# Performance work log

Hardware: AMD Instinct MI355X
Metric: run time of the kernel (lower is better)

The kernel has to match this reference:

```python
import jax, jax.numpy as jnp
import numpy as np

B, D, H, O, E, K = 16384, 3072, 128, 10, 8, 2


def setup_inputs() -> dict:
    key = jax.random.key(0)
    ks = jax.random.split(key, 9)
    s_d = 1.0 / np.sqrt(D)
    s_h = 1.0 / np.sqrt(H)
    return {
        "x": jax.random.normal(ks[0], (B, D), dtype=jnp.float32),
        "gate_w": jax.random.uniform(ks[1], (D, E), jnp.float32, -s_d, s_d),
        "gate_b": jnp.zeros((E,), jnp.float32),
        "w1": jax.random.uniform(ks[2], (E, D, H), jnp.float32, -s_d, s_d),
        "b1": jax.random.uniform(ks[3], (E, H), jnp.float32, -s_d, s_d),
        "w2": jax.random.uniform(ks[4], (E, H, H), jnp.float32, -s_h, s_h),
        "b2": jax.random.uniform(ks[5], (E, H), jnp.float32, -s_h, s_h),
        "w3": jax.random.uniform(ks[6], (E, H, O), jnp.float32, -s_h, s_h),
        "b3": jax.random.uniform(ks[7], (E, O), jnp.float32, -s_h, s_h),
    }


def reference(x, gate_w, gate_b, w1, b1, w2, b2, w3, b3):
    # Gate: scores [B, E]
    scores = x @ gate_w + gate_b
    _, topk_idx = jax.lax.top_k(scores, K)          # [B, K]
    mask = jax.nn.one_hot(topk_idx, E, dtype=scores.dtype).sum(axis=-2)  # [B, E] 0/1
    weights = jax.nn.softmax(scores, axis=-1) * mask
    weights = weights / (weights.sum(axis=-1, keepdims=True) + 1e-8)

    # Compute all experts (dropout is identity in eval mode)
    h1 = jax.nn.relu(jnp.einsum('bd,edh->beh', x, w1) + b1)   # [B, E, H]
    h2 = jax.nn.relu(jnp.einsum('beh,ehg->beg', h1, w2) + b2)  # [B, E, H]
    out = jnp.einsum('beh,eho->beo', h2, w3) + b3              # [B, E, O]

    y = jnp.einsum('be,beo->bo', weights, out)                 # [B, O]
    return y
```

## Files before the change

### kernel.cpp

```cpp
#include <hip/hip_runtime.h>
#include <hip/hip_bf16.h>

#define B_ROWS 16384
#define D_DIM  3072
#define H_DIM  128
#define O_DIM  10
#define E_NUM  8

typedef __hip_bfloat16 bf16;
typedef __attribute__((ext_vector_type(8))) short short8;
typedef __attribute__((ext_vector_type(4))) float floatx4;

__global__ void transpose_bf16_kernel(const float* __restrict__ in,
                                      bf16* __restrict__ out, int R, int C) {
    int e = blockIdx.z;
    const float* inp = in + (size_t)e * R * C;
    bf16* outp = out + (size_t)e * R * C;
    __shared__ float tile[32][33];
    int tx = threadIdx.x;
    int ty = threadIdx.y;
    int r0 = blockIdx.x * 32, c0 = blockIdx.y * 32;
#pragma unroll
    for (int i = 0; i < 4; i++)
        tile[ty + i * 8][tx] = inp[(size_t)(r0 + ty + i * 8) * C + c0 + tx];
    __syncthreads();
#pragma unroll
    for (int i = 0; i < 4; i++)
        outp[(size_t)(c0 + ty + i * 8) * R + r0 + tx] =
            __float2bfloat16(tile[tx][ty + i * 8]);
}

__global__ __launch_bounds__(256) void gate_w_reorder_kernel(
    const float* __restrict__ gw, float* __restrict__ gwr)
{
    int tid = blockIdx.x * 256 + threadIdx.x;
    int j = tid >> 9, rem = tid & 511;
    int k = rem >> 6, l = rem & 63;
    float4 v = *(const float4*)&gw[(size_t)(j * 256 + l * 4) * 8 + k * 4];
    *(float4*)&gwr[(size_t)tid * 4] = v;
}

__global__ __launch_bounds__(256, 4) void gate_kernel(
    const float* __restrict__ x, const float* __restrict__ gwr,
    const float* __restrict__ gate_b, bf16* __restrict__ x_bf16,
    int* __restrict__ rowlist, float* __restrict__ wlist, int* __restrict__ gcnt)
{
    __shared__ int   eidx[8][2];
    __shared__ float ew[8][2];
    __shared__ int   lcnt[E_NUM], gbase[E_NUM];

    int t = threadIdx.x, w = t >> 6, l = t & 63;
    int rowblk = blockIdx.x * 8;
    int r0 = rowblk + w * 2;

    float4 accA[2], accB[2];
#pragma unroll
    for (int r = 0; r < 2; r++) {
        accA[r] = (float4){0.f, 0.f, 0.f, 0.f};
        accB[r] = (float4){0.f, 0.f, 0.f, 0.f};
    }

    const float* xr0 = x + (size_t)r0 * D_DIM;
    const float* xr1 = x + (size_t)(r0 + 1) * D_DIM;
    int dl = l * 4;

    float4 xv[2], xn[2];
    xv[0] = *(const float4*)&xr0[dl];
    xv[1] = *(const float4*)&xr1[dl];

#pragma unroll 1
    for (int j = 0; j < 12; j++) {
        int dd = j * 256 + dl;
        const float4* gwp = (const float4*)(gwr + (size_t)j * 2048 + dl);
        float4 g[8];
#pragma unroll
        for (int k = 0; k < 8; k++) g[k] = gwp[k * 64];
        if (j < 11) {
            xn[0] = *(const float4*)&xr0[dd + 256];
            xn[1] = *(const float4*)&xr1[dd + 256];
        }
#pragma unroll
        for (int r = 0; r < 2; r++) {
            float4 xvv = xv[r];
            size_t xi = (size_t)(r0 + r) * D_DIM + dd;
            union { bf16 h[4]; uint2 v; } pk;
            pk.h[0] = __float2bfloat16(xvv.x);
            pk.h[1] = __float2bfloat16(xvv.y);
            pk.h[2] = __float2bfloat16(xvv.z);
            pk.h[3] = __float2bfloat16(xvv.w);
            *(uint2*)&x_bf16[xi] = pk.v;
            accA[r].x += xvv.x * g[0].x + xvv.y * g[2].x + xvv.z * g[4].x + xvv.w * g[6].x;
            accA[r].y += xvv.x * g[0].y + xvv.y * g[2].y + xvv.z * g[4].y + xvv.w * g[6].y;
            accA[r].z += xvv.x * g[0].z + xvv.y * g[2].z + xvv.z * g[4].z + xvv.w * g[6].z;
            accA[r].w += xvv.x * g[0].w + xvv.y * g[2].w + xvv.z * g[4].w + xvv.w * g[6].w;
            accB[r].x += xvv.x * g[1].x + xvv.y * g[3].x + xvv.z * g[5].x + xvv.w * g[7].x;
            accB[r].y += xvv.x * g[1].y + xvv.y * g[3].y + xvv.z * g[5].y + xvv.w * g[7].y;
            accB[r].z += xvv.x * g[1].z + xvv.y * g[3].z + xvv.z * g[5].z + xvv.w * g[7].z;
            accB[r].w += xvv.x * g[1].w + xvv.y * g[3].w + xvv.z * g[5].w + xvv.w * g[7].w;
        }
        xv[0] = xn[0];
        xv[1] = xn[1];
    }

#pragma unroll
    for (int r = 0; r < 2; r++) {
        float s[8] = {accA[r].x, accA[r].y, accA[r].z, accA[r].w,
                      accB[r].x, accB[r].y, accB[r].z, accB[r].w};
#pragma unroll
        for (int e = 0; e < 8; e++) {
            float v = s[e];
#pragma unroll
            for (int off = 1; off < 64; off <<= 1) v += __shfl_xor(v, off, 64);
            s[e] = v;
        }
        accA[r] = (float4){s[0], s[1], s[2], s[3]};
        accB[r] = (float4){s[4], s[5], s[6], s[7]};
    }

    if (l == 0) {
#pragma unroll
        for (int r = 0; r < 2; r++) {
            float s[8] = {accA[r].x, accA[r].y, accA[r].z, accA[r].w,
                          accB[r].x, accB[r].y, accB[r].z, accB[r].w};
#pragma unroll
            for (int e = 0; e < 8; e++) s[e] += gate_b[e];
            int i1 = 0; float m1 = s[0];
#pragma unroll
            for (int e = 1; e < 8; e++) if (s[e] > m1) { m1 = s[e]; i1 = e; }
            int i2 = -1; float m2 = -1e30f;
#pragma unroll
            for (int e = 0; e < 8; e++)
                if (e != i1 && s[e] > m2) { m2 = s[e]; i2 = e; }
            float S = 0.0f;
#pragma unroll
            for (int e = 0; e < 8; e++) S += expf(s[e] - m1);
            float p1 = expf(s[i1] - m1) / S;
            float p2 = expf(m2 - m1) / S;
            float denom = p1 + p2 + 1e-8f;
            eidx[w * 2 + r][0] = i1; ew[w * 2 + r][0] = p1 / denom;
            eidx[w * 2 + r][1] = i2; ew[w * 2 + r][1] = p2 / denom;
        }
    }
    __syncthreads();
    if (t < 8) lcnt[t] = 0;
    __syncthreads();
    int my_e = 0, my_lp = 0, my_rl = 0, my_sl = 0;
    if (t < 16) {
        my_rl = t >> 1; my_sl = t & 1;
        my_e = eidx[my_rl][my_sl];
        my_lp = atomicAdd(&lcnt[my_e], 1);
    }
    __syncthreads();
    if (t < 8) gbase[t] = atomicAdd(&gcnt[t], lcnt[t]);
    __syncthreads();
    if (t < 16) {
        int pos = gbase[my_e] + my_lp;
        rowlist[my_e * B_ROWS + pos] = rowblk + my_rl;
        wlist[my_e * B_ROWS + pos]   = ew[my_rl][my_sl];
    }
}

__global__ __launch_bounds__(512, 4) void gemm1_kernel(
    const bf16* __restrict__ xb, const bf16* __restrict__ w1t,
    const float* __restrict__ b1, const int* __restrict__ rowlist,
    const int* __restrict__ gcnt, bf16* __restrict__ h1buf)
{
    int e = blockIdx.y;
    int cnt = gcnt[e];
    int t0 = blockIdx.x * 64;
    if (t0 >= cnt) return;
    int mcnt = cnt - t0; if (mcnt > 64) mcnt = 64;

    __shared__ bf16 Ab[2][64][72];
    __shared__ bf16 Bb[2][128][72];
    __shared__ int rows_s[64];

    int t = threadIdx.x, w = t >> 6, l = t & 63;
    if (t < 64) {
        int rr = (t < mcnt) ? t : (mcnt - 1);
        rows_s[t] = rowlist[e * B_ROWS + t0 + rr];
    }
    __syncthreads();

    const bf16* w1base = w1t + (size_t)e * H_DIM * D_DIM;
    int ra = t >> 3, off8 = (t & 7) * 8;
    const bf16* aS  = xb + (size_t)rows_s[ra] * D_DIM + off8;
    const bf16* bS0 = w1base + (size_t)ra * D_DIM + off8;
    const bf16* bS1 = w1base + (size_t)(64 + ra) * D_DIM + off8;

    uint4 pa  = *(const uint4*)aS;
    uint4 pb0 = *(const uint4*)bS0;
    uint4 pb1 = *(const uint4*)bS1;

    int mb = (w & 3) * 16, nb = (w >> 2) * 64;

    floatx4 acc[4];
#pragma unroll
    for (int ni = 0; ni < 4; ni++) acc[ni] = (floatx4){0.f, 0.f, 0.f, 0.f};

    const int NKB = D_DIM / 64;
    for (int kb = 0; kb < NKB; kb++) {
        int bs = kb & 1;
        *(uint4*)&Ab[bs][ra][off8]      = pa;
        *(uint4*)&Bb[bs][ra][off8]      = pb0;
        *(uint4*)&Bb[bs][64 + ra][off8] = pb1;
        __syncthreads();
        if (kb + 1 < NKB) {
            int k0 = (kb + 1) * 64;
            pa  = *(const uint4*)(aS + k0);
            pb0 = *(const uint4*)(bS0 + k0);
            pb1 = *(const uint4*)(bS1 + k0);
        }
#pragma unroll
        for (int kc = 0; kc < 64; kc += 32) {
            short8 af = *(const short8*)&Ab[bs][mb + (l & 15)][kc + (l >> 4) * 8];
            short8 bfr[4];
#pragma unroll
            for (int ni = 0; ni < 4; ni++)
                bfr[ni] = *(const short8*)&Bb[bs][nb + ni * 16 + (l & 15)][kc + (l >> 4) * 8];
#pragma unroll
            for (int ni = 0; ni < 4; ni++)
                acc[ni] = __builtin_amdgcn_mfma_f32_16x16x32_bf16(af, bfr[ni], acc[ni], 0, 0, 0);
        }
    }

#pragma unroll
    for (int r = 0; r < 4; r++) {
        int row = mb + (l >> 4) * 4 + r;
        if (row < mcnt) {
#pragma unroll
            for (int ni = 0; ni < 4; ni++) {
                int col = nb + ni * 16 + (l & 15);
                float v = fmaxf(acc[ni][r] + b1[e * H_DIM + col], 0.0f);
                h1buf[(size_t)e * B_ROWS * H_DIM + (size_t)(t0 + row) * H_DIM + col] =
                    __float2bfloat16(v);
            }
        }
    }
}

__global__ __launch_bounds__(256) void gemm2c_kernel(
    const bf16* __restrict__ h1buf, const bf16* __restrict__ w2t,
    const float* __restrict__ b2, const float* __restrict__ w3,
    const float* __restrict__ b3, const int* __restrict__ rowlist,
    const float* __restrict__ wlist, const int* __restrict__ gcnt,
    float* __restrict__ y)
{
    int e = blockIdx.y;
    int cnt = gcnt[e];
    int t0 = blockIdx.x * 64;
    if (t0 >= cnt) return;
    int mcnt = cnt - t0; if (mcnt > 64) mcnt = 64;

    __shared__ bf16 h1s[64][136];
    __shared__ bf16 w2s[128][136];
    __shared__ bf16 w3ts[16 * 136];
    __shared__ float b2s[H_DIM], b3s[16], wts[64];
    __shared__ int rows_s[64];

    int t = threadIdx.x, w = t >> 6, l = t & 63;

    if (t < 64) {
        int rr = (t < mcnt) ? t : (mcnt - 1);
        rows_s[t] = rowlist[e * B_ROWS + t0 + rr];
        wts[t]    = wlist[e * B_ROWS + t0 + rr];
    }
    if (t < H_DIM) b2s[t] = b2[e * H_DIM + t];
    if (t < O_DIM) b3s[t] = b3[e * O_DIM + t];
    for (int idx = t; idx < H_DIM * O_DIM; idx += 256)
        w3ts[(idx % 10) * 136 + idx / 10] = __float2bfloat16(w3[(size_t)e * H_DIM * O_DIM + idx]);
    for (int idx = t; idx < 6 * 128; idx += 256)
        w3ts[(10 + idx / 128) * 136 + (idx % 128)] = __float2bfloat16(0.0f);

    {
        const bf16* h1base = h1buf + (size_t)e * B_ROWS * H_DIM + (size_t)t0 * H_DIM;
        int hend = mcnt * 16;
#pragma unroll
        for (int k = 0; k < 4; k++) {
            int si = t + 256 * k;
            if (si < hend)
                *(uint4*)&h1s[si >> 4][(si & 15) * 8] =
                    *(const uint4*)(h1base + (size_t)(si >> 4) * H_DIM + (si & 15) * 8);
        }
        const bf16* w2base = w2t + (size_t)e * H_DIM * H_DIM;
#pragma unroll
        for (int k = 0; k < 8; k++) {
            int si = t + 256 * k;
            *(uint4*)&w2s[si >> 4][(si & 15) * 8] =
                *(const uint4*)(w2base + (size_t)(si >> 4) * H_DIM + (si & 15) * 8);
        }
    }
    __syncthreads();

    int mb = (w & 1) * 32, nb = (w >> 1) * 64;
    floatx4 acc2[2][4];
#pragma unroll
    for (int mi = 0; mi < 2; mi++)
#pragma unroll
        for (int ni = 0; ni < 4; ni++) acc2[mi][ni] = (floatx4){0.f, 0.f, 0.f, 0.f};
#pragma unroll
    for (int kc = 0; kc < 128; kc += 32) {
        short8 af[2], bfr[4];
#pragma unroll
        for (int mi = 0; mi < 2; mi++)
            af[mi] = *(const short8*)&h1s[mb + mi * 16 + (l & 15)][kc + (l >> 4) * 8];
#pragma unroll
        for (int ni = 0; ni < 4; ni++)
            bfr[ni] = *(const short8*)&w2s[nb + ni * 16 + (l & 15)][kc + (l >> 4) * 8];
#pragma unroll
        for (int mi = 0; mi < 2; mi++)
#pragma unroll
            for (int ni = 0; ni < 4; ni++)
                acc2[mi][ni] = __builtin_amdgcn_mfma_f32_16x16x32_bf16(
                    af[mi], bfr[ni], acc2[mi][ni], 0, 0, 0);
    }
    __syncthreads();

    bf16* h2s = &h1s[0][0];
#pragma unroll
    for (int mi = 0; mi < 2; mi++)
#pragma unroll
        for (int r = 0; r < 4; r++) {
            int row = mb + mi * 16 + (l >> 4) * 4 + r;
#pragma unroll
            for (int ni = 0; ni < 4; ni++) {
                int col = nb + ni * 16 + (l & 15);
                float v = fmaxf(acc2[mi][ni][r] + b2s[col], 0.0f);
                h2s[row * 136 + col] = __float2bfloat16(v);
            }
        }
    __syncthreads();

    floatx4 acc3 = (floatx4){0.f, 0.f, 0.f, 0.f};
    int m3 = w * 16;
#pragma unroll
    for (int kc = 0; kc < 128; kc += 32) {
        short8 af  = *(const short8*)&h2s[(m3 + (l & 15)) * 136 + kc + (l >> 4) * 8];
        short8 bf3 = *(const short8*)&w3ts[(l & 15) * 136 + kc + (l >> 4) * 8];
        acc3 = __builtin_amdgcn_mfma_f32_16x16x32_bf16(af, bf3, acc3, 0, 0, 0);
    }
    int col = l & 15;
    if (col < O_DIM) {
#pragma unroll
        for (int r = 0; r < 4; r++) {
            int row = m3 + (l >> 4) * 4 + r;
            if (row < mcnt)
                atomicAdd(&y[(size_t)rows_s[row] * O_DIM + col],
                          wts[row] * (acc3[r] + b3s[col]));
        }
    }
}

extern "C" void kernel_launch(void* const* d_in, const int* in_sizes, int n_in,
                              void* d_out, int out_size, void* d_ws, size_t ws_size,
                              hipStream_t stream) {
    (void)in_sizes; (void)n_in; (void)ws_size;
    const float* x      = (const float*)d_in[0];
    const float* gate_w = (const float*)d_in[1];
    const float* gate_b = (const float*)d_in[2];
    const float* w1     = (const float*)d_in[3];
    const float* b1     = (const float*)d_in[4];
    const float* w2     = (const float*)d_in[5];
    const float* b2     = (const float*)d_in[6];
    const float* w3     = (const float*)d_in[7];
    const float* b3     = (const float*)d_in[8];
    float* y = (float*)d_out;

    char* ws = (char*)d_ws;
    size_t off = 0;
    auto alloc = [&](size_t bytes) {
        void* p = ws + off;
        off = (off + bytes + 255) & ~(size_t)255;
        return p;
    };
    bf16*  x_bf16  = (bf16*)alloc((size_t)B_ROWS * D_DIM * 2);
    bf16*  w1t     = (bf16*)alloc((size_t)E_NUM * H_DIM * D_DIM * 2);
    bf16*  w2t     = (bf16*)alloc((size_t)E_NUM * H_DIM * H_DIM * 2);
    bf16*  h1buf   = (bf16*)alloc((size_t)E_NUM * B_ROWS * H_DIM * 2);
    float* gwr     = (float*)alloc((size_t)D_DIM * E_NUM * 4);
    int*   rowlist = (int*)alloc((size_t)E_NUM * B_ROWS * 4);
    float* wlist   = (float*)alloc((size_t)E_NUM * B_ROWS * 4);
    int*   gcnt    = (int*)alloc(64);

    hipMemsetAsync(d_out, 0, (size_t)out_size * sizeof(float), stream);
    hipMemsetAsync(gcnt, 0, 64, stream);

    gate_w_reorder_kernel<<<D_DIM * E_NUM / 4 / 256, 256, 0, stream>>>(gate_w, gwr);
    transpose_bf16_kernel<<<dim3(D_DIM / 32, H_DIM / 32, E_NUM), dim3(32, 8), 0, stream>>>(
        w1, w1t, D_DIM, H_DIM);
    transpose_bf16_kernel<<<dim3(H_DIM / 32, H_DIM / 32, E_NUM), dim3(32, 8), 0, stream>>>(
        w2, w2t, H_DIM, H_DIM);
    gate_kernel<<<B_ROWS / 8, 256, 0, stream>>>(x, gwr, gate_b, x_bf16,
                                                rowlist, wlist, gcnt);
    gemm1_kernel<<<dim3(B_ROWS / 64, E_NUM), 512, 0, stream>>>(
        x_bf16, w1t, b1, rowlist, gcnt, h1buf);
    gemm2c_kernel<<<dim3(B_ROWS / 64, E_NUM), 256, 0, stream>>>(
        h1buf, w2t, b2, w3, b3, rowlist, wlist, gcnt, y);
}
```

Baseline: 467.3 us.

## Use async global-to-LDS loads, XOR-swizzled LDS, and 128-row tiles in gemm1

Rewrites the gemm1 main loop to use global_load_lds direct-to-LDS asynchronous copies instead of register-staged loads. LDS is stored unpadded with an XOR swizzle to avoid bank conflicts. Each block now covers 128 rows, so every wave does 2x4 MFMA tiles and reuses each B fragment more. The grid is flattened with the expert index in the low bits so consecutive blocks interleave experts, in both gemm1 and gemm2c. Risks include relying on async-load ordering with only __syncthreads for completion, and fewer blocks for load balancing.

After: 428.7 us. -8.3%, faster.

```diff
diff --git a/kernel.cpp b/kernel.cpp
--- a/kernel.cpp
+++ b/kernel.cpp
@@ -10,6 +10,12 @@
 typedef __hip_bfloat16 bf16;
 typedef __attribute__((ext_vector_type(8))) short short8;
 typedef __attribute__((ext_vector_type(4))) float floatx4;
+
+__device__ __forceinline__ void async_load16(const bf16* g, bf16* l) {
+    __builtin_amdgcn_global_load_lds(
+        (const __attribute__((address_space(1))) unsigned int*)(const void*)g,
+        (__attribute__((address_space(3))) unsigned int*)(void*)l, 16, 0, 0);
+}
 
 __global__ void transpose_bf16_kernel(const float* __restrict__ in,
                                       bf16* __restrict__ out, int R, int C) {
@@ -165,78 +171,97 @@
     const float* __restrict__ b1, const int* __restrict__ rowlist,
     const int* __restrict__ gcnt, bf16* __restrict__ h1buf)
 {
-    int e = blockIdx.y;
+    int e  = blockIdx.x & 7;
+    int bx = blockIdx.x >> 3;
     int cnt = gcnt[e];
-    int t0 = blockIdx.x * 64;
+    int t0 = bx * 128;
     if (t0 >= cnt) return;
-    int mcnt = cnt - t0; if (mcnt > 64) mcnt = 64;
-
-    __shared__ bf16 Ab[2][64][72];
-    __shared__ bf16 Bb[2][128][72];
-    __shared__ int rows_s[64];
+    int mcnt = cnt - t0; if (mcnt > 128) mcnt = 128;
+
+    __shared__ bf16 Ab[2][128 * 64];
+    __shared__ bf16 Bb[2][128 * 64];
+    __shared__ int rows_s[128];
 
     int t = threadIdx.x, w = t >> 6, l = t & 63;
-    if (t < 64) {
+    if (t < 128) {
         int rr = (t < mcnt) ? t : (mcnt - 1);
         rows_s[t] = rowlist[e * B_ROWS + t0 + rr];
     }
     __syncthreads();
 
     const bf16* w1base = w1t + (size_t)e * H_DIM * D_DIM;
-    int ra = t >> 3, off8 = (t & 7) * 8;
-    const bf16* aS  = xb + (size_t)rows_s[ra] * D_DIM + off8;
-    const bf16* bS0 = w1base + (size_t)ra * D_DIM + off8;
-    const bf16* bS1 = w1base + (size_t)(64 + ra) * D_DIM + off8;
-
-    uint4 pa  = *(const uint4*)aS;
-    uint4 pb0 = *(const uint4*)bS0;
-    uint4 pb1 = *(const uint4*)bS1;
-
-    int mb = (w & 3) * 16, nb = (w >> 2) * 64;
-
-    floatx4 acc[4];
-#pragma unroll
-    for (int ni = 0; ni < 4; ni++) acc[ni] = (floatx4){0.f, 0.f, 0.f, 0.f};
+    int sub = l >> 3;
+    int blk = (l & 7) ^ sub;
+    const bf16* aP0 = xb + (size_t)rows_s[w * 16 + sub]     * D_DIM + blk * 8;
+    const bf16* aP1 = xb + (size_t)rows_s[w * 16 + 8 + sub] * D_DIM + blk * 8;
+    const bf16* bP0 = w1base + (size_t)(w * 16 + sub)     * D_DIM + blk * 8;
+    const bf16* bP1 = w1base + (size_t)(w * 16 + 8 + sub) * D_DIM + blk * 8;
+    bf16* ldsA0 = &Ab[0][(2 * w) * 512], *ldsA1 = &Ab[0][(2 * w + 1) * 512];
+    bf16* ldsB0 = &Bb[0][(2 * w) * 512], *ldsB1 = &Bb[0][(2 * w + 1) * 512];
+
+    auto stage = [&](int bs, int kb) {
+        int k0 = kb * 64;
+        int boff = bs * 128 * 64;
+        async_load16(aP0 + k0, ldsA0 + boff);
+        async_load16(aP1 + k0, ldsA1 + boff);
+        async_load16(bP0 + k0, ldsB0 + boff);
+        async_load16(bP1 + k0, ldsB1 + boff);
+    };
+
+    int wr = w & 3, wc = w >> 2;
+    floatx4 acc[2][4];
+#pragma unroll
+    for (int mi = 0; mi < 2; mi++)
+#pragma unroll
+        for (int ni = 0; ni < 4; ni++) acc[mi][ni] = (floatx4){0.f, 0.f, 0.f, 0.f};
+
+    stage(0, 0);
 
     const int NKB = D_DIM / 64;
     for (int kb = 0; kb < NKB; kb++) {
         int bs = kb & 1;
-        *(uint4*)&Ab[bs][ra][off8]      = pa;
-        *(uint4*)&Bb[bs][ra][off8]      = pb0;
-        *(uint4*)&Bb[bs][64 + ra][off8] = pb1;
         __syncthreads();
-        if (kb + 1 < NKB) {
-            int k0 = (kb + 1) * 64;
-            pa  = *(const uint4*)(aS + k0);
-            pb0 = *(const uint4*)(bS0 + k0);
-            pb1 = *(const uint4*)(bS1 + k0);
-        }
-#pragma unroll
-        for (int kc = 0; kc < 64; kc += 32) {
-            short8 af = *(const short8*)&Ab[bs][mb + (l & 15)][kc + (l >> 4) * 8];
-            short8 bfr[4];
-#pragma unroll
-            for (int ni = 0; ni < 4; ni++)
-                bfr[ni] = *(const short8*)&Bb[bs][nb + ni * 16 + (l & 15)][kc + (l >> 4) * 8];
-#pragma unroll
-            for (int ni = 0; ni < 4; ni++)
-                acc[ni] = __builtin_amdgcn_mfma_f32_16x16x32_bf16(af, bfr[ni], acc[ni], 0, 0, 0);
-        }
-    }
-
-#pragma unroll
-    for (int r = 0; r < 4; r++) {
-        int row = mb + (l >> 4) * 4 + r;
-        if (row < mcnt) {
+        if (kb + 1 < NKB) stage(bs ^ 1, kb + 1);
+#pragma unroll
+        for (int kc8 = 0; kc8 < 8; kc8 += 4) {
+            int c = kc8 + (l >> 4);
+            int swz = (c ^ (l & 7)) * 8;
+            short8 af[2], bfr[4];
+#pragma unroll
+            for (int mi = 0; mi < 2; mi++) {
+                int R = wr * 32 + mi * 16 + (l & 15);
+                af[mi] = *(const short8*)&Ab[bs][R * 64 + swz];
+            }
 #pragma unroll
             for (int ni = 0; ni < 4; ni++) {
-                int col = nb + ni * 16 + (l & 15);
-                float v = fmaxf(acc[ni][r] + b1[e * H_DIM + col], 0.0f);
-                h1buf[(size_t)e * B_ROWS * H_DIM + (size_t)(t0 + row) * H_DIM + col] =
-                    __float2bfloat16(v);
+                int C = wc * 64 + ni * 16 + (l & 15);
+                bfr[ni] = *(const short8*)&Bb[bs][C * 64 + swz];
             }
-        }
-    }
+#pragma unroll
+            for (int mi = 0; mi < 2; mi++)
+#pragma unroll
+                for (int ni = 0; ni < 4; ni++)
+                    acc[mi][ni] = __builtin_amdgcn_mfma_f32_16x16x32_bf16(
+                        af[mi], bfr[ni], acc[mi][ni], 0, 0, 0);
+        }
+    }
+
+    const float* b1e = b1 + e * H_DIM;
+#pragma unroll
+    for (int mi = 0; mi < 2; mi++)
+#pragma unroll
+        for (int r = 0; r < 4; r++) {
+            int row = wr * 32 + mi * 16 + (l >> 4) * 4 + r;
+            if (row < mcnt) {
+#pragma unroll
+                for (int ni = 0; ni < 4; ni++) {
+                    int col = wc * 64 + ni * 16 + (l & 15);
+                    float v = fmaxf(acc[mi][ni][r] + b1e[col], 0.0f);
+                    h1buf[(size_t)e * B_ROWS * H_DIM + (size_t)(t0 + row) * H_DIM + col] =
+                        __float2bfloat16(v);
+                }
+            }
+        }
 }
 
 __global__ __launch_bounds__(256) void gemm2c_kernel(
@@ -246,9 +271,10 @@
     const float* __restrict__ wlist, const int* __restrict__ gcnt,
     float* __restrict__ y)
 {
-    int e = blockIdx.y;
+    int e  = blockIdx.x & 7;
+    int bx = blockIdx.x >> 3;
     int cnt = gcnt[e];
-    int t0 = blockIdx.x * 64;
+    int t0 = bx * 64;
     if (t0 >= cnt) return;
     int mcnt = cnt - t0; if (mcnt > 64) mcnt = 64;
 
@@ -392,8 +418,8 @@
         w2, w2t, H_DIM, H_DIM);
     gate_kernel<<<B_ROWS / 8, 256, 0, stream>>>(x, gwr, gate_b, x_bf16,
                                                 rowlist, wlist, gcnt);
-    gemm1_kernel<<<dim3(B_ROWS / 64, E_NUM), 512, 0, stream>>>(
+    gemm1_kernel<<<(B_ROWS / 128) * E_NUM, 512, 0, stream>>>(
         x_bf16, w1t, b1, rowlist, gcnt, h1buf);
-    gemm2c_kernel<<<dim3(B_ROWS / 64, E_NUM), 256, 0, stream>>>(
+    gemm2c_kernel<<<(B_ROWS / 64) * E_NUM, 256, 0, stream>>>(
         h1buf, w2t, b2, w3, b3, rowlist, wlist, gcnt, y);
 }
```
